# Kernel tuning notes

Measured on AMD Instinct MI355X. Metric: run time of the kernel, lower is better.

Reference implementation:

```python
import jax, jax.numpy as jnp
import numpy as np
from jax import lax

N = 8388608
NG = 1024
TAU = 0.1
GAMMA = 0.05
MAX_ITERS = 30
EPS = 1e-9


def setup_inputs() -> dict:
    key = jax.random.key(0)
    k1, k2, k3 = jax.random.split(key, 3)
    y_raw = jax.random.uniform(k1, (N,), dtype=jnp.float32)
    y_real = jax.random.uniform(k2, (N,), dtype=jnp.float32)
    group_ids = jax.random.randint(k3, (N,), 0, NG, dtype=jnp.int32)
    return {"y_raw": y_raw, "y_real": y_real, "group_ids": group_ids, "n_groups": NG}


def reference(y_raw, y_real, group_ids, n_groups):
    y_real = jnp.maximum(y_real, EPS)
    l = (1.0 - TAU) * y_real          # per-element lower box bound
    u = (1.0 + TAU) * y_real          # per-element upper box bound
    y_clipped = jnp.clip(y_raw, l, u)
    w = 1.0 / jnp.maximum(y_real, 1e-9)

    seg_sum = lambda v: jax.ops.segment_sum(v, group_ids, num_segments=n_groups)

    n_g = seg_sum(jnp.ones_like(y_raw))            # [G] group sizes
    L = (1.0 - GAMMA) * n_g
    U = (1.0 + GAMMA) * n_g
    S0 = seg_sum(w * y_clipped)                    # [G] ratio sums at alpha=0
    feasible = (S0 >= L) & (S0 <= U)

    # per-group bracketing interval for alpha
    alo = jax.ops.segment_min((l - y_raw) * w, group_ids, num_segments=n_groups) - 1.0
    ahi = jax.ops.segment_max((u - y_raw) * w, group_ids, num_segments=n_groups) + 1.0
    nonempty = n_g > 0
    alo = jnp.where(nonempty, alo, 0.0)            # guard empty groups (inf/-inf)
    ahi = jnp.where(nonempty, ahi, 0.0)
    T = jnp.where(S0 < L, L, U)                    # [G] bisection target

    def step(carry, _):
        lo, hi, _ = carry
        mid = 0.5 * (lo + hi)                                    # [G]
        y_mid = jnp.clip(y_raw + mid[group_ids] / w, l, u)       # [N]
        Smid = seg_sum(w * y_mid)                                # [G]
        lo = jnp.where(Smid < T, mid, lo)
        hi = jnp.where(Smid >= T, mid, hi)
        return (lo, hi, mid), None

    (lo, hi, mid), _ = lax.scan(step, (alo, ahi, alo), None, length=MAX_ITERS)
    y_bis = jnp.clip(y_raw + mid[group_ids] / w, l, u)           # last iterate y_mid
    return jnp.where(feasible[group_ids], y_clipped, y_bis)
```

## Files before the change

### kernel.cpp

```cpp
#include <hip/hip_runtime.h>

#define N_ELEM   8388608
#define NGROUPS  1024
#define EPSF     1e-9f
#define MAX_ITERS 30

__device__ __forceinline__ unsigned enc_f(float f) {
    unsigned u = __float_as_uint(f);
    return (u & 0x80000000u) ? ~u : (u | 0x80000000u);
}
__device__ __forceinline__ float dec_f(unsigned e) {
    unsigned u = (e & 0x80000000u) ? (e ^ 0x80000000u) : ~e;
    return __uint_as_float(u);
}

__global__ __launch_bounds__(NGROUPS) void k_init(float* gsum, unsigned* gcnt,
                                                  unsigned* gmn, unsigned* gmx) {
    int g = threadIdx.x;
    gsum[g] = 0.0f;
    gcnt[g] = 0u;
    gmn[g]  = 0xFFFFFFFFu;
    gmx[g]  = 0u;
}

__global__ __launch_bounds__(1024) void k_stats(const float4* __restrict__ yraw4,
                                                const float4* __restrict__ yreal4,
                                                const int4*   __restrict__ gid4,
                                                float4*       __restrict__ out4,
                                                float* gsum, unsigned* gcnt,
                                                unsigned* gmn, unsigned* gmx, int n4) {
    __shared__ float    s_sum[NGROUPS];
    __shared__ unsigned s_cnt[NGROUPS];
    __shared__ unsigned s_mn[NGROUPS];
    __shared__ unsigned s_mx[NGROUPS];
    int t = threadIdx.x;
    for (int g = t; g < NGROUPS; g += blockDim.x) {
        s_sum[g] = 0.0f; s_cnt[g] = 0u; s_mn[g] = 0xFFFFFFFFu; s_mx[g] = 0u;
    }
    __syncthreads();

    int stride = gridDim.x * blockDim.x;
    for (int i = blockIdx.x * blockDim.x + t; i < n4; i += stride) {
        float4 yr = yraw4[i];
        float4 ye = yreal4[i];
        int4   gg = gid4[i];
        float yrs[4] = { yr.x, yr.y, yr.z, yr.w };
        float yes[4] = { ye.x, ye.y, ye.z, ye.w };
        int   gs[4]  = { gg.x, gg.y, gg.z, gg.w };
        float oc[4];
#pragma unroll
        for (int j = 0; j < 4; ++j) {
            float yraw = yrs[j];
            float yrc  = fmaxf(yes[j], EPSF);
            float l = 0.9f * yrc;
            float u = 1.1f * yrc;
            float yclip = fminf(fmaxf(yraw, l), u);
            oc[j] = yclip;
            float w = 1.0f / yrc;
            float s  = w * yclip;
            float a0 = (l - yraw) * w;
            float a1 = (u - yraw) * w;
            int g = gs[j];
            atomicAdd(&s_sum[g], s);
            atomicAdd(&s_cnt[g], 1u);
            atomicMin(&s_mn[g], enc_f(a0));
            atomicMax(&s_mx[g], enc_f(a1));
        }
        out4[i] = make_float4(oc[0], oc[1], oc[2], oc[3]);
    }
    __syncthreads();
    for (int g = t; g < NGROUPS; g += blockDim.x) {
        atomicAdd(&gsum[g], s_sum[g]);
        atomicAdd(&gcnt[g], s_cnt[g]);
        atomicMin(&gmn[g], s_mn[g]);
        atomicMax(&gmx[g], s_mx[g]);
    }
}

__global__ __launch_bounds__(NGROUPS) void k_group(const float* gsum, const unsigned* gcnt,
                                                   const unsigned* gmn, const unsigned* gmx,
                                                   unsigned* feas, float* gT, float* glo,
                                                   float* ghi, float* galpha, unsigned* gbase,
                                                   unsigned* gcur, unsigned* total) {
    __shared__ unsigned s_scan[NGROUPS];
    int g = threadIdx.x;
    unsigned c = gcnt[g];
    float n  = (float)c;
    float S0 = gsum[g];
    float L = 0.95f * n;
    float U = 1.05f * n;
    unsigned f = (S0 >= L && S0 <= U) ? 1u : 0u;
    float alo, ahi;
    if (c == 0u) { alo = 0.0f; ahi = 0.0f; }
    else { alo = dec_f(gmn[g]) - 1.0f; ahi = dec_f(gmx[g]) + 1.0f; }
    feas[g]   = f;
    gT[g]     = (S0 < L) ? L : U;
    glo[g]    = alo;
    ghi[g]    = ahi;
    galpha[g] = 0.0f;

    unsigned v = f ? 0u : c;
    s_scan[g] = v;
    for (int off = 1; off < NGROUPS; off <<= 1) {
        __syncthreads();
        unsigned tmp = (g >= off) ? s_scan[g - off] : 0u;
        __syncthreads();
        s_scan[g] += tmp;
    }
    __syncthreads();
    unsigned incl = s_scan[g];
    unsigned base = incl - v;
    gbase[g] = base;
    gcur[g]  = base;
    if (g == NGROUPS - 1) *total = incl;
}

__global__ __launch_bounds__(256) void k_compact(const int4* __restrict__ gid4,
                                                 const unsigned* __restrict__ feas,
                                                 unsigned* gcur, const unsigned* total,
                                                 unsigned* cidx, unsigned* cgid,
                                                 unsigned capacity, int n4) {
    if (*total == 0u) return;
    __shared__ unsigned s_feas[NGROUPS];
    for (int g = threadIdx.x; g < NGROUPS; g += blockDim.x) s_feas[g] = feas[g];
    __syncthreads();
    int stride = gridDim.x * blockDim.x;
    for (int i = blockIdx.x * blockDim.x + threadIdx.x; i < n4; i += stride) {
        int4 gg = gid4[i];
        int gs[4] = { gg.x, gg.y, gg.z, gg.w };
#pragma unroll
        for (int j = 0; j < 4; ++j) {
            int g = gs[j];
            if (!s_feas[g]) {
                unsigned pos = atomicAdd(&gcur[g], 1u);
                if (pos < capacity) {
                    cidx[pos] = (unsigned)(4 * i + j);
                    cgid[pos] = (unsigned)g;
                }
            }
        }
    }
}

#define CAPC 8064
__global__ __launch_bounds__(256) void k_bisect(const float* __restrict__ y_raw,
                                                const float* __restrict__ y_real,
                                                const unsigned* feas, const unsigned* gcnt,
                                                const unsigned* gbase, const float* gT,
                                                const float* glo_a, const float* ghi_a,
                                                float* galpha, const unsigned* __restrict__ cidx,
                                                unsigned capacity) {
    int g = blockIdx.x;
    if (feas[g]) return;
    __shared__ float2 cache[CAPC];
    __shared__ double s_part[4];
    __shared__ float  s_mid;
    unsigned base = gbase[g];
    unsigned cnt  = gcnt[g];
    if (base >= capacity) cnt = 0;
    else if (cnt > capacity - base) cnt = capacity - base;
    int t = threadIdx.x;
    for (unsigned i = t; i < cnt && i < CAPC; i += 256u) {
        unsigned idx = cidx[base + i];
        cache[i] = make_float2(y_raw[idx], y_real[idx]);
    }
    __syncthreads();
    float lo = glo_a[g], hi = ghi_a[g], T = gT[g];
    float mid = lo;
    for (int it = 0; it < MAX_ITERS; ++it) {
        if (t == 0) s_mid = 0.5f * (lo + hi);
        __syncthreads();
        float m = s_mid;
        double part = 0.0;
        for (unsigned i = t; i < cnt; i += 256u) {
            float yraw, ye;
            if (i < CAPC) { float2 v = cache[i]; yraw = v.x; ye = v.y; }
            else { unsigned idx = cidx[base + i]; yraw = y_raw[idx]; ye = y_real[idx]; }
            float yrc = fmaxf(ye, EPSF);
            float l = 0.9f * yrc;
            float u = 1.1f * yrc;
            float w = 1.0f / yrc;
            float ym = fminf(fmaxf(yraw + m / w, l), u);
            part += (double)(w * ym);
        }
#pragma unroll
        for (int off = 32; off > 0; off >>= 1) part += __shfl_down(part, off, 64);
        if ((t & 63) == 0) s_part[t >> 6] = part;
        __syncthreads();
        if (t == 0) {
            float Smid = (float)(s_part[0] + s_part[1] + s_part[2] + s_part[3]);
            if (Smid < T) lo = m; else hi = m;
        }
        mid = m;
        __syncthreads();
    }
    if (t == 0) galpha[g] = mid;
}

__global__ __launch_bounds__(256) void k_fixup(const float* __restrict__ y_raw,
                                               const float* __restrict__ y_real,
                                               const unsigned* __restrict__ cidx,
                                               const unsigned* __restrict__ cgid,
                                               const float* galpha, const unsigned* total,
                                               float* __restrict__ out, unsigned capacity) {
    unsigned tot = *total;
    if (tot > capacity) tot = capacity;
    unsigned stride = gridDim.x * blockDim.x;
    for (unsigned i = blockIdx.x * blockDim.x + threadIdx.x; i < tot; i += stride) {
        unsigned idx = cidx[i];
        unsigned g   = cgid[i];
        float yraw = y_raw[idx];
        float yrc  = fmaxf(y_real[idx], EPSF);
        float l = 0.9f * yrc;
        float u = 1.1f * yrc;
        float w = 1.0f / yrc;
        float a = galpha[g];
        out[idx] = fminf(fmaxf(yraw + a / w, l), u);
    }
}

extern "C" void kernel_launch(void* const* d_in, const int* in_sizes, int n_in,
                              void* d_out, int out_size, void* d_ws, size_t ws_size,
                              hipStream_t stream) {
    const float* y_raw  = (const float*)d_in[0];
    const float* y_real = (const float*)d_in[1];
    const int*   gid    = (const int*)d_in[2];
    float* out = (float*)d_out;
    const int n  = in_sizes[0];
    const int n4 = n / 4;

    char* ws = (char*)d_ws;
    float*    gsum   = (float*)(ws + 0);
    unsigned* gcnt   = (unsigned*)(ws + 4096);
    unsigned* gmn    = (unsigned*)(ws + 8192);
    unsigned* gmx    = (unsigned*)(ws + 12288);
    unsigned* feas   = (unsigned*)(ws + 16384);
    float*    gT     = (float*)(ws + 20480);
    float*    glo    = (float*)(ws + 24576);
    float*    ghi    = (float*)(ws + 28672);
    float*    galpha = (float*)(ws + 32768);
    unsigned* gbase  = (unsigned*)(ws + 36864);
    unsigned* gcur   = (unsigned*)(ws + 40960);
    unsigned* total  = (unsigned*)(ws + 45056);
    unsigned* cidx   = (unsigned*)(ws + 49152);
    size_t cap64 = (ws_size > 49152) ? (ws_size - 49152) / 8 : 0;
    if (cap64 > (size_t)n) cap64 = (size_t)n;
    unsigned capacity = (unsigned)cap64;
    unsigned* cgid = cidx + capacity;

    k_init<<<1, NGROUPS, 0, stream>>>(gsum, gcnt, gmn, gmx);
    k_stats<<<256, 1024, 0, stream>>>((const float4*)y_raw, (const float4*)y_real,
                                      (const int4*)gid, (float4*)out,
                                      gsum, gcnt, gmn, gmx, n4);
    k_group<<<1, NGROUPS, 0, stream>>>(gsum, gcnt, gmn, gmx, feas, gT, glo, ghi,
                                       galpha, gbase, gcur, total);
    k_compact<<<512, 256, 0, stream>>>((const int4*)gid, feas, gcur, total,
                                       cidx, cgid, capacity, n4);
    k_bisect<<<NGROUPS, 256, 0, stream>>>(y_raw, y_real, feas, gcnt, gbase, gT,
                                          glo, ghi, galpha, cidx, capacity);
    k_fixup<<<512, 256, 0, stream>>>(y_raw, y_real, cidx, cgid, galpha, total,
                                     out, capacity);
}
```

Before: 168.7 us.

## Pack group count and fixed-point sum into one 64-bit atomic, defer min/max

The stats pass now accumulates count and a fixed-point ratio sum in a single 64-bit shared atomic per element, instead of four separate shared atomics. The per-group min/max bracket is computed only for infeasible groups, inside the compaction pass, which now also reads the value arrays but only for vectors touching infeasible groups. The stats kernel also switches from a grid-stride loop to one block per 4096 float4s with all loads issued before compute. The fixed-point sum trades float accumulation for integer rounding at 2^-30 resolution, which could flip a feasibility decision near a bound, and the 49-bit sum field could overflow for very large groups.

```diff
diff --git a/kernel.cpp b/kernel.cpp
--- a/kernel.cpp
+++ b/kernel.cpp
@@ -1,9 +1,12 @@
 #include <hip/hip_runtime.h>
 
-#define N_ELEM   8388608
 #define NGROUPS  1024
 #define EPSF     1e-9f
 #define MAX_ITERS 30
+#define SUM_MASK ((1ull << 49) - 1)
+#define CNT_SHIFT 49
+#define FIX_SCALE 1073741824.0f
+#define FIX_INV   (1.0 / 1073741824.0)
 
 __device__ __forceinline__ unsigned enc_f(float f) {
     unsigned u = __float_as_uint(f);
@@ -14,39 +17,40 @@
     return __uint_as_float(u);
 }
 
-__global__ __launch_bounds__(NGROUPS) void k_init(float* gsum, unsigned* gcnt,
+__global__ __launch_bounds__(NGROUPS) void k_init(unsigned long long* gpack,
                                                   unsigned* gmn, unsigned* gmx) {
     int g = threadIdx.x;
-    gsum[g] = 0.0f;
-    gcnt[g] = 0u;
-    gmn[g]  = 0xFFFFFFFFu;
-    gmx[g]  = 0u;
+    gpack[g] = 0ull;
+    gmn[g]   = 0xFFFFFFFFu;
+    gmx[g]   = 0u;
 }
 
 __global__ __launch_bounds__(1024) void k_stats(const float4* __restrict__ yraw4,
                                                 const float4* __restrict__ yreal4,
                                                 const int4*   __restrict__ gid4,
                                                 float4*       __restrict__ out4,
-                                                float* gsum, unsigned* gcnt,
-                                                unsigned* gmn, unsigned* gmx, int n4) {
-    __shared__ float    s_sum[NGROUPS];
-    __shared__ unsigned s_cnt[NGROUPS];
-    __shared__ unsigned s_mn[NGROUPS];
-    __shared__ unsigned s_mx[NGROUPS];
+                                                unsigned long long* gpack, int n4) {
+    __shared__ unsigned long long s_pk[NGROUPS];
     int t = threadIdx.x;
-    for (int g = t; g < NGROUPS; g += blockDim.x) {
-        s_sum[g] = 0.0f; s_cnt[g] = 0u; s_mn[g] = 0xFFFFFFFFu; s_mx[g] = 0u;
-    }
-    __syncthreads();
-
-    int stride = gridDim.x * blockDim.x;
-    for (int i = blockIdx.x * blockDim.x + t; i < n4; i += stride) {
-        float4 yr = yraw4[i];
-        float4 ye = yreal4[i];
-        int4   gg = gid4[i];
-        float yrs[4] = { yr.x, yr.y, yr.z, yr.w };
-        float yes[4] = { ye.x, ye.y, ye.z, ye.w };
-        int   gs[4]  = { gg.x, gg.y, gg.z, gg.w };
+    s_pk[t] = 0ull;
+    __syncthreads();
+
+    int base = blockIdx.x * 4096;
+    float4 yr[4], ye[4];
+    int4   gg[4];
+    bool   ok[4];
+#pragma unroll
+    for (int k = 0; k < 4; ++k) {
+        int i = base + k * 1024 + t;
+        ok[k] = (i < n4);
+        if (ok[k]) { yr[k] = yraw4[i]; ye[k] = yreal4[i]; gg[k] = gid4[i]; }
+    }
+#pragma unroll
+    for (int k = 0; k < 4; ++k) {
+        if (!ok[k]) continue;
+        float yrs[4] = { yr[k].x, yr[k].y, yr[k].z, yr[k].w };
+        float yes[4] = { ye[k].x, ye[k].y, ye[k].z, ye[k].w };
+        int   gs[4]  = { gg[k].x, gg[k].y, gg[k].z, gg[k].w };
         float oc[4];
 #pragma unroll
         for (int j = 0; j < 4; ++j) {
@@ -56,47 +60,32 @@
             float u = 1.1f * yrc;
             float yclip = fminf(fmaxf(yraw, l), u);
             oc[j] = yclip;
-            float w = 1.0f / yrc;
-            float s  = w * yclip;
-            float a0 = (l - yraw) * w;
-            float a1 = (u - yraw) * w;
-            int g = gs[j];
-            atomicAdd(&s_sum[g], s);
-            atomicAdd(&s_cnt[g], 1u);
-            atomicMin(&s_mn[g], enc_f(a0));
-            atomicMax(&s_mx[g], enc_f(a1));
-        }
-        out4[i] = make_float4(oc[0], oc[1], oc[2], oc[3]);
-    }
-    __syncthreads();
-    for (int g = t; g < NGROUPS; g += blockDim.x) {
-        atomicAdd(&gsum[g], s_sum[g]);
-        atomicAdd(&gcnt[g], s_cnt[g]);
-        atomicMin(&gmn[g], s_mn[g]);
-        atomicMax(&gmx[g], s_mx[g]);
-    }
-}
-
-__global__ __launch_bounds__(NGROUPS) void k_group(const float* gsum, const unsigned* gcnt,
-                                                   const unsigned* gmn, const unsigned* gmx,
-                                                   unsigned* feas, float* gT, float* glo,
-                                                   float* ghi, float* galpha, unsigned* gbase,
+            float s = yclip / yrc;
+            unsigned long long pk = (1ull << CNT_SHIFT)
+                + (unsigned long long)__float2uint_rn(s * FIX_SCALE);
+            atomicAdd(&s_pk[gs[j]], pk);
+        }
+        out4[base + k * 1024 + t] = make_float4(oc[0], oc[1], oc[2], oc[3]);
+    }
+    __syncthreads();
+    if (s_pk[t] != 0ull) atomicAdd(&gpack[t], s_pk[t]);
+}
+
+__global__ __launch_bounds__(NGROUPS) void k_group(const unsigned long long* gpack,
+                                                   unsigned* feas, float* gT,
+                                                   float* galpha, unsigned* gbase,
                                                    unsigned* gcur, unsigned* total) {
     __shared__ unsigned s_scan[NGROUPS];
     int g = threadIdx.x;
-    unsigned c = gcnt[g];
+    unsigned long long pk = gpack[g];
+    unsigned c = (unsigned)(pk >> CNT_SHIFT);
+    float S0 = (float)((double)(pk & SUM_MASK) * FIX_INV);
     float n  = (float)c;
-    float S0 = gsum[g];
     float L = 0.95f * n;
     float U = 1.05f * n;
     unsigned f = (S0 >= L && S0 <= U) ? 1u : 0u;
-    float alo, ahi;
-    if (c == 0u) { alo = 0.0f; ahi = 0.0f; }
-    else { alo = dec_f(gmn[g]) - 1.0f; ahi = dec_f(gmx[g]) + 1.0f; }
     feas[g]   = f;
     gT[g]     = (S0 < L) ? L : U;
-    glo[g]    = alo;
-    ghi[g]    = ahi;
     galpha[g] = 0.0f;
 
     unsigned v = f ? 0u : c;
@@ -115,29 +104,57 @@
     if (g == NGROUPS - 1) *total = incl;
 }
 
-__global__ __launch_bounds__(256) void k_compact(const int4* __restrict__ gid4,
-                                                 const unsigned* __restrict__ feas,
-                                                 unsigned* gcur, const unsigned* total,
-                                                 unsigned* cidx, unsigned* cgid,
-                                                 unsigned capacity, int n4) {
+__global__ __launch_bounds__(256) void k_mmc(const float4* __restrict__ yraw4,
+                                             const float4* __restrict__ yreal4,
+                                             const int4*   __restrict__ gid4,
+                                             const unsigned* __restrict__ feas,
+                                             unsigned* gcur, const unsigned* total,
+                                             unsigned* gmn, unsigned* gmx,
+                                             unsigned* cidx, unsigned* cgid,
+                                             unsigned capacity, int n4) {
     if (*total == 0u) return;
     __shared__ unsigned s_feas[NGROUPS];
-    for (int g = threadIdx.x; g < NGROUPS; g += blockDim.x) s_feas[g] = feas[g];
+    __shared__ unsigned s_mn[NGROUPS];
+    __shared__ unsigned s_mx[NGROUPS];
+    for (int g = threadIdx.x; g < NGROUPS; g += blockDim.x) {
+        s_feas[g] = feas[g]; s_mn[g] = 0xFFFFFFFFu; s_mx[g] = 0u;
+    }
     __syncthreads();
     int stride = gridDim.x * blockDim.x;
     for (int i = blockIdx.x * blockDim.x + threadIdx.x; i < n4; i += stride) {
         int4 gg = gid4[i];
         int gs[4] = { gg.x, gg.y, gg.z, gg.w };
+        bool any = !s_feas[gs[0]] || !s_feas[gs[1]] || !s_feas[gs[2]] || !s_feas[gs[3]];
+        if (!any) continue;
+        float4 yr = yraw4[i];
+        float4 ye = yreal4[i];
+        float yrs[4] = { yr.x, yr.y, yr.z, yr.w };
+        float yes[4] = { ye.x, ye.y, ye.z, ye.w };
 #pragma unroll
         for (int j = 0; j < 4; ++j) {
             int g = gs[j];
-            if (!s_feas[g]) {
-                unsigned pos = atomicAdd(&gcur[g], 1u);
-                if (pos < capacity) {
-                    cidx[pos] = (unsigned)(4 * i + j);
-                    cgid[pos] = (unsigned)g;
-                }
+            if (s_feas[g]) continue;
+            float yraw = yrs[j];
+            float yrc  = fmaxf(yes[j], EPSF);
+            float l = 0.9f * yrc;
+            float u = 1.1f * yrc;
+            float w = 1.0f / yrc;
+            float a0 = (l - yraw) * w;
+            float a1 = (u - yraw) * w;
+            atomicMin(&s_mn[g], enc_f(a0));
+            atomicMax(&s_mx[g], enc_f(a1));
+            unsigned pos = atomicAdd(&gcur[g], 1u);
+            if (pos < capacity) {
+                cidx[pos] = (unsigned)(4 * i + j);
+                cgid[pos] = (unsigned)g;
             }
+        }
+    }
+    __syncthreads();
+    for (int g = threadIdx.x; g < NGROUPS; g += blockDim.x) {
+        if (!s_feas[g]) {
+            atomicMin(&gmn[g], s_mn[g]);
+            atomicMax(&gmx[g], s_mx[g]);
         }
     }
 }
@@ -145,10 +162,12 @@
 #define CAPC 8064
 __global__ __launch_bounds__(256) void k_bisect(const float* __restrict__ y_raw,
                                                 const float* __restrict__ y_real,
-                                                const unsigned* feas, const unsigned* gcnt,
+                                                const unsigned* feas,
+                                                const unsigned long long* gpack,
                                                 const unsigned* gbase, const float* gT,
-                                                const float* glo_a, const float* ghi_a,
-                                                float* galpha, const unsigned* __restrict__ cidx,
+                                                const unsigned* gmn, const unsigned* gmx,
+                                                float* galpha,
+                                                const unsigned* __restrict__ cidx,
                                                 unsigned capacity) {
     int g = blockIdx.x;
     if (feas[g]) return;
@@ -156,7 +175,7 @@
     __shared__ double s_part[4];
     __shared__ float  s_mid;
     unsigned base = gbase[g];
-    unsigned cnt  = gcnt[g];
+    unsigned cnt  = (unsigned)(gpack[g] >> CNT_SHIFT);
     if (base >= capacity) cnt = 0;
     else if (cnt > capacity - base) cnt = capacity - base;
     int t = threadIdx.x;
@@ -165,7 +184,9 @@
         cache[i] = make_float2(y_raw[idx], y_real[idx]);
     }
     __syncthreads();
-    float lo = glo_a[g], hi = ghi_a[g], T = gT[g];
+    float lo = dec_f(gmn[g]) - 1.0f;
+    float hi = dec_f(gmx[g]) + 1.0f;
+    float T  = gT[g];
     float mid = lo;
     for (int it = 0; it < MAX_ITERS; ++it) {
         if (t == 0) s_mid = 0.5f * (lo + hi);
@@ -230,34 +251,32 @@
     const int n4 = n / 4;
 
     char* ws = (char*)d_ws;
-    float*    gsum   = (float*)(ws + 0);
-    unsigned* gcnt   = (unsigned*)(ws + 4096);
+    unsigned long long* gpack = (unsigned long long*)(ws + 0);
     unsigned* gmn    = (unsigned*)(ws + 8192);
     unsigned* gmx    = (unsigned*)(ws + 12288);
     unsigned* feas   = (unsigned*)(ws + 16384);
     float*    gT     = (float*)(ws + 20480);
-    float*    glo    = (float*)(ws + 24576);
-    float*    ghi    = (float*)(ws + 28672);
-    float*    galpha = (float*)(ws + 32768);
-    unsigned* gbase  = (unsigned*)(ws + 36864);
-    unsigned* gcur   = (unsigned*)(ws + 40960);
-    unsigned* total  = (unsigned*)(ws + 45056);
-    unsigned* cidx   = (unsigned*)(ws + 49152);
-    size_t cap64 = (ws_size > 49152) ? (ws_size - 49152) / 8 : 0;
+    float*    galpha = (float*)(ws + 24576);
+    unsigned* gbase  = (unsigned*)(ws + 28672);
+    unsigned* gcur   = (unsigned*)(ws + 32768);
+    unsigned* total  = (unsigned*)(ws + 36864);
+    unsigned* cidx   = (unsigned*)(ws + 40960);
+    size_t cap64 = (ws_size > 40960) ? (ws_size - 40960) / 8 : 0;
     if (cap64 > (size_t)n) cap64 = (size_t)n;
     unsigned capacity = (unsigned)cap64;
     unsigned* cgid = cidx + capacity;
 
-    k_init<<<1, NGROUPS, 0, stream>>>(gsum, gcnt, gmn, gmx);
-    k_stats<<<256, 1024, 0, stream>>>((const float4*)y_raw, (const float4*)y_real,
-                                      (const int4*)gid, (float4*)out,
-                                      gsum, gcnt, gmn, gmx, n4);
-    k_group<<<1, NGROUPS, 0, stream>>>(gsum, gcnt, gmn, gmx, feas, gT, glo, ghi,
-                                       galpha, gbase, gcur, total);
-    k_compact<<<512, 256, 0, stream>>>((const int4*)gid, feas, gcur, total,
-                                       cidx, cgid, capacity, n4);
-    k_bisect<<<NGROUPS, 256, 0, stream>>>(y_raw, y_real, feas, gcnt, gbase, gT,
-                                          glo, ghi, galpha, cidx, capacity);
+    int nb_stats = (n4 + 4095) / 4096;
+
+    k_init<<<1, NGROUPS, 0, stream>>>(gpack, gmn, gmx);
+    k_stats<<<nb_stats, 1024, 0, stream>>>((const float4*)y_raw, (const float4*)y_real,
+                                           (const int4*)gid, (float4*)out, gpack, n4);
+    k_group<<<1, NGROUPS, 0, stream>>>(gpack, feas, gT, galpha, gbase, gcur, total);
+    k_mmc<<<512, 256, 0, stream>>>((const float4*)y_raw, (const float4*)y_real,
+                                   (const int4*)gid, feas, gcur, total,
+                                   gmn, gmx, cidx, cgid, capacity, n4);
+    k_bisect<<<NGROUPS, 256, 0, stream>>>(y_raw, y_real, feas, gpack, gbase, gT,
+                                          gmn, gmx, galpha, cidx, capacity);
     k_fixup<<<512, 256, 0, stream>>>(y_raw, y_real, cidx, cgid, galpha, total,
                                      out, capacity);
 }
```

New measurement: 150.7 us. 10.7% less time.
